# Kernel optimization log

Hardware: AMD Instinct MI355X
Metric: run time of the kernel (lower is better)

The kernel has to match this reference:

```python
import jax, jax.numpy as jnp
import numpy as np

NHEAD = 8
TEMP = 1.0
LAMB = 1.0
G_MIN = 1e-3


def _linear(x, w, b):
    # torch nn.Linear convention: w is (out, in)
    return x @ w.T + b


def _ln(x, s, b):
    m = x.mean(-1, keepdims=True)
    v = ((x - m) ** 2).mean(-1, keepdims=True)
    return (x - m) / jnp.sqrt(v + 1e-5) * s + b


def _gate(x, w, b):
    # UncertaintyGate, gate_mode='mu_times_evi'
    nig = _linear(x, w, b)  # [B, L, 4]
    mu = nig[..., 0]
    v = jax.nn.softplus(nig[..., 1]) + 1e-6
    alpha = jax.nn.softplus(nig[..., 2]) + 1.0 + 1e-6
    beta = jax.nn.softplus(nig[..., 3]) + 1e-6
    sigma_e2 = beta / (v * (alpha - 1.0))
    g = jax.nn.sigmoid(mu) * jnp.exp(-LAMB * sigma_e2)
    return jnp.clip(g, G_MIN, 1.0)  # [B, L]


def _cross_attn(q, k, v, gate, mask):
    B, Lq, D = q.shape
    Lk = k.shape[1]
    hd = D // NHEAD
    q = q.reshape(B, Lq, NHEAD, hd).transpose(0, 2, 1, 3)
    k = k.reshape(B, Lk, NHEAD, hd).transpose(0, 2, 1, 3)
    v = v.reshape(B, Lk, NHEAD, hd).transpose(0, 2, 1, 3)
    scores = jnp.einsum('bhqd,bhkd->bhqk', q, k) / jnp.sqrt(jnp.float32(hd))
    scores = scores + jnp.log(gate + 1e-9)[:, None, None, :]  # per-key log-gate bias
    scores = jnp.where(mask[:, None, None, :] == 0, -1e9, scores)
    attn = jax.nn.softmax(scores / TEMP, axis=-1)
    out = jnp.einsum('bhqk,bhkd->bhqd', attn, v)
    return out.transpose(0, 2, 1, 3).reshape(B, Lq, D)


def _ffn(x, w1, b1, w2, b2):
    return _linear(jax.nn.gelu(_linear(x, w1, b1), approximate=False), w2, b2)


def setup_inputs() -> dict:
    key = jax.random.key(0)
    ks = iter(jax.random.split(key, 64))
    D, B, Ld, Lp = 512, 16, 256, 1024
    def w(shape, s=0.02):
        return jax.random.normal(next(ks), shape, jnp.float32) * s
    inp = {
        'h_d': jax.random.normal(next(ks), (B, Ld, D), jnp.float32),
        'h_p': jax.random.normal(next(ks), (B, Lp, D), jnp.float32),
        'gd_w': w((4, D)), 'gd_b': jnp.zeros((4,), jnp.float32),
        'gp_w': w((4, D)), 'gp_b': jnp.zeros((4,), jnp.float32),
        'wqd_w': w((D, D)), 'wqd_b': jnp.zeros((D,), jnp.float32),
        'wkp_w': w((D, D)), 'wkp_b': jnp.zeros((D,), jnp.float32),
        'wvp_w': w((D, D)), 'wvp_b': jnp.zeros((D,), jnp.float32),
        'wqp_w': w((D, D)), 'wqp_b': jnp.zeros((D,), jnp.float32),
        'wkd_w': w((D, D)), 'wkd_b': jnp.zeros((D,), jnp.float32),
        'wvd_w': w((D, D)), 'wvd_b': jnp.zeros((D,), jnp.float32),
        'od_w': w((D, D)), 'od_b': jnp.zeros((D,), jnp.float32),
        'op_w': w((D, D)), 'op_b': jnp.zeros((D,), jnp.float32),
        'fd1_w': w((4 * D, D)), 'fd1_b': jnp.zeros((4 * D,), jnp.float32),
        'fd2_w': w((D, 4 * D)), 'fd2_b': jnp.zeros((D,), jnp.float32),
        'fp1_w': w((4 * D, D)), 'fp1_b': jnp.zeros((4 * D,), jnp.float32),
        'fp2_w': w((D, 4 * D)), 'fp2_b': jnp.zeros((D,), jnp.float32),
        'nd1_s': jnp.ones((D,), jnp.float32), 'nd1_b': jnp.zeros((D,), jnp.float32),
        'nd2_s': jnp.ones((D,), jnp.float32), 'nd2_b': jnp.zeros((D,), jnp.float32),
        'np1_s': jnp.ones((D,), jnp.float32), 'np1_b': jnp.zeros((D,), jnp.float32),
        'np2_s': jnp.ones((D,), jnp.float32), 'np2_b': jnp.zeros((D,), jnp.float32),
        'mask_d': jnp.ones((B, Ld), jnp.int32),
        'mask_p': jnp.ones((B, Lp), jnp.int32),
    }
    return inp


def reference(h_d, h_p, gd_w, gd_b, gp_w, gp_b, wqd_w, wqd_b, wkp_w, wkp_b,
              wvp_w, wvp_b, wqp_w, wqp_b, wkd_w, wkd_b, wvd_w, wvd_b,
              od_w, od_b, op_w, op_b, fd1_w, fd1_b, fd2_w, fd2_b,
              fp1_w, fp1_b, fp2_w, fp2_b, nd1_s, nd1_b, nd2_s, nd2_b,
              np1_s, np1_b, np2_s, np2_b, mask_d, mask_p):
    # gates are computed from the ORIGINAL inputs
    g_d = _gate(h_d, gd_w, gd_b)
    g_p = _gate(h_p, gp_w, gp_b)
    # drug attends to protein
    attn_d = _cross_attn(_linear(h_d, wqd_w, wqd_b),
                         _linear(h_p, wkp_w, wkp_b),
                         _linear(h_p, wvp_w, wvp_b), g_p, mask_p)
    h_d = _ln(h_d + _linear(attn_d, od_w, od_b), nd1_s, nd1_b)
    # protein attends to UPDATED drug (matches original control flow)
    attn_p = _cross_attn(_linear(h_p, wqp_w, wqp_b),
                         _linear(h_d, wkd_w, wkd_b),
                         _linear(h_d, wvd_w, wvd_b), g_d, mask_d)
    h_p = _ln(h_p + _linear(attn_p, op_w, op_b), np1_s, np1_b)
    h_d = _ln(h_d + _ffn(h_d, fd1_w, fd1_b, fd2_w, fd2_b), nd2_s, nd2_b)
    h_p = _ln(h_p + _ffn(h_p, fp1_w, fp1_b, fp2_w, fp2_b), np2_s, np2_b)
    return (h_d, h_p)
```

## Files before the change

kernel.cpp:

```cpp
#include <hip/hip_runtime.h>

typedef float f32x4 __attribute__((ext_vector_type(4)));
typedef short bfrag __attribute__((ext_vector_type(8)));
typedef short s16x8 __attribute__((ext_vector_type(8)));
typedef unsigned short u16;

__device__ __forceinline__ u16 f2bf(float f) {
  union { float f; unsigned u; } x; x.f = f;
  unsigned r = x.u + 0x7fffu + ((x.u >> 16) & 1u);
  return (u16)(r >> 16);
}
__device__ __forceinline__ float bf2f(u16 v) {
  union { unsigned u; float f; } x; x.u = ((unsigned)v) << 16;
  return x.f;
}

__device__ __forceinline__ void g2l16(const void* g, void* l) {
  void* gnc = const_cast<void*>(g);
  __builtin_amdgcn_global_load_lds((__attribute__((address_space(1))) void*)gnc,
                                   (__attribute__((address_space(3))) void*)l, 16, 0, 0);
}

__device__ __forceinline__ f32x4 mfma16(bfrag a, bfrag b, f32x4 c) {
  asm volatile("v_mfma_f32_16x16x32_bf16 %0, %1, %2, %0" : "+v"(c) : "v"(a), "v"(b));
  return c;
}

__device__ __forceinline__ float wred_sum(float s) {
  #pragma unroll
  for (int o = 32; o; o >>= 1) s += __shfl_xor(s, o);
  return s;
}

struct CvtArgs {
  const float* s[14];
  u16* d[14];
  int eb[14];
};

__global__ __launch_bounds__(256) void cvt_all(CvtArgs a) {
  const int blk = blockIdx.x;
  int base = 0;
  const float* sp = a.s[0];
  u16* dp = a.d[0];
  #pragma unroll
  for (int i = 0; i < 13; ++i) {
    if (blk >= a.eb[i]) { base = a.eb[i]; sp = a.s[i + 1]; dp = a.d[i + 1]; }
  }
  const size_t gi = ((size_t)(blk - base) * 256 + threadIdx.x) * 4;
  float4 f = *(const float4*)(sp + gi);
  ushort4 o;
  o.x = f2bf(f.x); o.y = f2bf(f.y); o.z = f2bf(f.z); o.w = f2bf(f.w);
  *(ushort4*)(dp + gi) = o;
}

__device__ __forceinline__ float softplus_s(float x) {
  return fmaxf(x, 0.f) + log1pf(expf(-fabsf(x)));
}

__global__ __launch_bounds__(256) void gate_k(
    const float* __restrict__ hd, const float* __restrict__ hp,
    const float* __restrict__ wd, const float* __restrict__ bd,
    const float* __restrict__ wp, const float* __restrict__ bp,
    float* __restrict__ lgd, float* __restrict__ lgp, int mdTok) {
  const int lane = threadIdx.x & 63, wv = threadIdx.x >> 6;
  size_t tok = (size_t)blockIdx.x * 4 + wv;
  const float* h; const float* w4; const float* b4; float* lg;
  if (tok < (size_t)mdTok) { h = hd; w4 = wd; b4 = bd; lg = lgd; }
  else { h = hp; w4 = wp; b4 = bp; lg = lgp; tok -= mdTok; }
  const float* x = h + tok * 512;
  float s0 = 0.f, s1 = 0.f, s2 = 0.f, s3 = 0.f;
  #pragma unroll
  for (int i = 0; i < 8; ++i) {
    int c = (i << 6) + lane;
    float xv = x[c];
    s0 += xv * w4[c];
    s1 += xv * w4[512 + c];
    s2 += xv * w4[1024 + c];
    s3 += xv * w4[1536 + c];
  }
  s0 = wred_sum(s0); s1 = wred_sum(s1); s2 = wred_sum(s2); s3 = wred_sum(s3);
  if (lane == 0) {
    float mu = s0 + b4[0];
    float va = softplus_s(s1 + b4[1]) + 1e-6f;
    float al = softplus_s(s2 + b4[2]) + 1.f + 1e-6f;
    float be = softplus_s(s3 + b4[3]) + 1e-6f;
    float se2 = be / (va * (al - 1.f));
    float g = (1.f / (1.f + expf(-mu))) * expf(-se2);
    g = fminf(fmaxf(g, 1e-3f), 1.f);
    lg[tok] = logf(g + 1e-9f);
  }
}

template <int RES, int OUT>
__global__ __launch_bounds__(256) void ln_k(const void* __restrict__ resv,
                                            const u16* __restrict__ y,
                                            const float* __restrict__ sc,
                                            const float* __restrict__ bi,
                                            void* __restrict__ outv) {
  const int lane = threadIdx.x & 63, w = threadIdx.x >> 6;
  const size_t row = (size_t)blockIdx.x * 4 + w;
  const int c0 = lane * 8;
  float v[8];
  s16x8 yv = *(const s16x8*)(y + row * 512 + c0);
  if constexpr (RES == 0) {
    const float* rf = (const float*)resv + row * 512 + c0;
    float4 r0 = *(const float4*)rf, r1 = *(const float4*)(rf + 4);
    v[0] = r0.x; v[1] = r0.y; v[2] = r0.z; v[3] = r0.w;
    v[4] = r1.x; v[5] = r1.y; v[6] = r1.z; v[7] = r1.w;
  } else {
    s16x8 rv = *(const s16x8*)((const u16*)resv + row * 512 + c0);
    #pragma unroll
    for (int i = 0; i < 8; ++i) v[i] = bf2f((u16)rv[i]);
  }
  float s = 0.f;
  #pragma unroll
  for (int i = 0; i < 8; ++i) { v[i] += bf2f((u16)yv[i]); s += v[i]; }
  s = wred_sum(s);
  float m = s * (1.f / 512.f);
  float s2 = 0.f;
  #pragma unroll
  for (int i = 0; i < 8; ++i) { float d = v[i] - m; s2 += d * d; }
  s2 = wred_sum(s2);
  float inv = rsqrtf(s2 * (1.f / 512.f) + 1e-5f);
  float4 sc0 = *(const float4*)(sc + c0), sc1 = *(const float4*)(sc + c0 + 4);
  float4 bi0 = *(const float4*)(bi + c0), bi1 = *(const float4*)(bi + c0 + 4);
  float scv[8] = {sc0.x, sc0.y, sc0.z, sc0.w, sc1.x, sc1.y, sc1.z, sc1.w};
  float biv[8] = {bi0.x, bi0.y, bi0.z, bi0.w, bi1.x, bi1.y, bi1.z, bi1.w};
  float o[8];
  #pragma unroll
  for (int i = 0; i < 8; ++i) o[i] = (v[i] - m) * inv * scv[i] + biv[i];
  if constexpr (OUT == 0) {
    float* of = (float*)outv + row * 512 + c0;
    *(float4*)of = float4{o[0], o[1], o[2], o[3]};
    *(float4*)(of + 4) = float4{o[4], o[5], o[6], o[7]};
  } else {
    s16x8 ov;
    #pragma unroll
    for (int i = 0; i < 8; ++i) ov[i] = (short)f2bf(o[i]);
    *(s16x8*)((u16*)outv + row * 512 + c0) = ov;
  }
}

template <int KT>
__global__ __launch_bounds__(256) void flash_k(
    const u16* __restrict__ Q, const u16* __restrict__ Kv,
    const u16* __restrict__ Vt, const float* __restrict__ logg,
    const int* __restrict__ mask, u16* __restrict__ Out,
    int Lq, int Lk, float scale) {
  __shared__ __align__(16) u16 Kl[KT * 64];
  __shared__ __align__(16) u16 Vl[64 * KT];
  __shared__ __align__(16) u16 Pl[64 * (KT + 8)];
  const int tid = threadIdx.x;
  const int lane = tid & 63, wv = tid >> 6;
  const int lr = lane & 15, lg4 = lane >> 4;
  const int bh = blockIdx.z;
  const int b = bh >> 3, h = bh & 7;
  const int q0 = blockIdx.x * 64;

  bfrag af[2];
  {
    const u16* qrow = Q + (size_t)(b * Lq + q0 + wv * 16 + lr) * 512 + h * 64;
    af[0] = *(const bfrag*)(qrow + lg4 * 8);
    af[1] = *(const bfrag*)(qrow + 32 + lg4 * 8);
  }
  float mreg[4] = {-3e38f, -3e38f, -3e38f, -3e38f};
  float lreg[4] = {0.f, 0.f, 0.f, 0.f};
  f32x4 Oa[4] = {};
  const float* lgb = logg + (size_t)b * Lk;
  const int* mkb = mask + (size_t)b * Lk;

  const int NKT = Lk / KT;
  for (int t = 0; t < NKT; ++t) {
    const int k0 = t * KT;
    __syncthreads();
    {
      const char* kb = (const char*)(Kv + (size_t)(b * Lk + k0) * 512 + h * 64);
      #pragma unroll
      for (int r = 0; r < KT / 32; ++r) {
        int o = r * 4096 + tid * 16;
        int rr = o >> 7, cd = (o >> 4) & 7;
        int cs = cd ^ (rr & 7);
        g2l16(kb + (size_t)rr * 1024 + cs * 16, (char*)Kl + o);
      }
      const char* vb = (const char*)(Vt + (size_t)bh * 64 * Lk + k0);
      #pragma unroll
      for (int r = 0; r < KT / 32; ++r) {
        int o = r * 4096 + tid * 16;
        int rr = o >> 8, cd = (o >> 4) & 15;
        int cs = (cd & 8) | ((cd & 7) ^ (rr & 7));
        g2l16(vb + (size_t)rr * (Lk * 2) + cs * 16, (char*)Vl + o);
      }
    }
    __syncthreads();

    f32x4 sa[KT / 16];
    #pragma unroll
    for (int n = 0; n < KT / 16; ++n) {
      sa[n] = f32x4{0.f, 0.f, 0.f, 0.f};
      int row = n * 16 + lr;
      #pragma unroll
      for (int ks = 0; ks < 2; ++ks) {
        bfrag kf = *(const bfrag*)(Kl + row * 64 + (((ks * 4 + lg4) ^ (row & 7)) * 8));
        sa[n] = mfma16(af[ks], kf, sa[n]);
      }
    }
    asm volatile("s_nop 7\n\ts_nop 7");

    float pv[KT / 16][4];
    float nm[4] = {-3e38f, -3e38f, -3e38f, -3e38f};
    #pragma unroll
    for (int n = 0; n < KT / 16; ++n) {
      int kk = k0 + n * 16 + lr;
      float lgv = lgb[kk];
      int mkv = mkb[kk];
      #pragma unroll
      for (int e = 0; e < 4; ++e) {
        float tv = mkv ? fmaf(sa[n][e], scale, lgv) : -1e9f;
        pv[n][e] = tv;
        nm[e] = fmaxf(nm[e], tv);
      }
    }
    float fac[4], rs[4];
    #pragma unroll
    for (int e = 0; e < 4; ++e) {
      nm[e] = fmaxf(nm[e], __shfl_xor(nm[e], 1));
      nm[e] = fmaxf(nm[e], __shfl_xor(nm[e], 2));
      nm[e] = fmaxf(nm[e], __shfl_xor(nm[e], 4));
      nm[e] = fmaxf(nm[e], __shfl_xor(nm[e], 8));
      nm[e] = fmaxf(nm[e], mreg[e]);
      fac[e] = __expf(mreg[e] - nm[e]);
      mreg[e] = nm[e];
      rs[e] = 0.f;
    }
    #pragma unroll
    for (int n = 0; n < KT / 16; ++n)
      #pragma unroll
      for (int e = 0; e < 4; ++e) {
        float p = __expf(pv[n][e] - nm[e]);
        pv[n][e] = p;
        rs[e] += p;
      }
    #pragma unroll
    for (int e = 0; e < 4; ++e) {
      rs[e] += __shfl_xor(rs[e], 1);
      rs[e] += __shfl_xor(rs[e], 2);
      rs[e] += __shfl_xor(rs[e], 4);
      rs[e] += __shfl_xor(rs[e], 8);
      lreg[e] = lreg[e] * fac[e] + rs[e];
    }
    #pragma unroll
    for (int n2 = 0; n2 < 4; ++n2)
      #pragma unroll
      for (int e = 0; e < 4; ++e) Oa[n2][e] *= fac[e];

    {
      int prow = wv * 16 + lg4 * 4;
      #pragma unroll
      for (int n = 0; n < KT / 16; ++n)
        #pragma unroll
        for (int e = 0; e < 4; ++e)
          Pl[(prow + e) * (KT + 8) + n * 16 + lr] = f2bf(pv[n][e]);
    }
    #pragma unroll
    for (int ks = 0; ks < KT / 32; ++ks) {
      bfrag pf = *(const bfrag*)(Pl + (wv * 16 + lr) * (KT + 8) + (ks * 4 + lg4) * 8);
      #pragma unroll
      for (int n2 = 0; n2 < 4; ++n2) {
        int vrow = n2 * 16 + lr;
        int ch = ks * 4 + lg4;
        int chs = (ch & 8) | ((ch & 7) ^ (vrow & 7));
        bfrag vf = *(const bfrag*)(Vl + vrow * KT + chs * 8);
        Oa[n2] = mfma16(pf, vf, Oa[n2]);
      }
    }
  }
  asm volatile("s_nop 7\n\ts_nop 7");

  float inv[4];
  #pragma unroll
  for (int e = 0; e < 4; ++e) inv[e] = 1.f / lreg[e];
  u16* ob = Out + (size_t)(b * Lq + q0 + wv * 16 + lg4 * 4) * 512 + h * 64;
  #pragma unroll
  for (int n2 = 0; n2 < 4; ++n2)
    #pragma unroll
    for (int e = 0; e < 4; ++e)
      ob[(size_t)e * 512 + n2 * 16 + lr] = f2bf(Oa[n2][e] * inv[e]);
}

template <int FM, int FN, int EPI>
__global__ __launch_bounds__(256) void gemm_k(
    const u16* __restrict__ A, const u16* __restrict__ W,
    const float* __restrict__ bias, void* __restrict__ C,
    int K, int lda, int ldw, int ldc, int NB, int TR) {
  constexpr int BM = 2 * FM * 16;
  constexpr int BN = 2 * FN * 16;
  __shared__ __align__(16) u16 Al[BM * 64];
  __shared__ __align__(16) u16 Wl[BN * 64];
  const int tid = threadIdx.x;
  const int qq = gridDim.x >> 3;
  const int wg = (blockIdx.x & 7) * qq + (blockIdx.x >> 3);
  const int bx = wg % NB, by = wg / NB;
  const int row0 = by * BM, col0 = bx * BN;
  const int lane = tid & 63, wv = tid >> 6;
  const int wr = wv >> 1, wc = wv & 1;
  const int rowW = wr * FM * 16, colW = wc * FN * 16;
  const int lr = lane & 15, lg4 = lane >> 4;

  const u16* aSrc[BM / 32];
  const u16* wSrc[BN / 32];
  int aDst[BM / 32], wDst[BN / 32];
  #pragma unroll
  for (int r = 0; r < BM / 32; ++r) {
    int o = r * 4096 + tid * 16;
    int arow = o >> 7, cd = (o >> 4) & 7, cs = cd ^ (arow & 7);
    aSrc[r] = A + (size_t)(row0 + arow) * lda + cs * 8;
    aDst[r] = o;
  }
  #pragma unroll
  for (int r = 0; r < BN / 32; ++r) {
    int o = r * 4096 + tid * 16;
    int wrow = o >> 7, cd = (o >> 4) & 7, cs = cd ^ (wrow & 7);
    wSrc[r] = W + (size_t)(col0 + wrow) * ldw + cs * 8;
    wDst[r] = o;
  }
  int aOff[FM][2], wOff[FN][2];
  #pragma unroll
  for (int m = 0; m < FM; ++m) {
    int rowi = rowW + m * 16 + lr;
    #pragma unroll
    for (int ks = 0; ks < 2; ++ks)
      aOff[m][ks] = rowi * 64 + (((ks * 4 + lg4) ^ (rowi & 7)) * 8);
  }
  #pragma unroll
  for (int n = 0; n < FN; ++n) {
    int rowi = colW + n * 16 + lr;
    #pragma unroll
    for (int ks = 0; ks < 2; ++ks)
      wOff[n][ks] = rowi * 64 + (((ks * 4 + lg4) ^ (rowi & 7)) * 8);
  }

  f32x4 acc[FM][FN] = {};

  for (int k0 = 0; k0 < K; k0 += 64) {
    #pragma unroll
    for (int r = 0; r < BM / 32; ++r) g2l16(aSrc[r] + k0, (char*)Al + aDst[r]);
    #pragma unroll
    for (int r = 0; r < BN / 32; ++r) g2l16(wSrc[r] + k0, (char*)Wl + wDst[r]);
    __syncthreads();
    #pragma unroll
    for (int ks = 0; ks < 2; ++ks) {
      bfrag af[FM], wf[FN];
      #pragma unroll
      for (int m = 0; m < FM; ++m) af[m] = *(const bfrag*)(Al + aOff[m][ks]);
      #pragma unroll
      for (int n = 0; n < FN; ++n) wf[n] = *(const bfrag*)(Wl + wOff[n][ks]);
      #pragma unroll
      for (int m = 0; m < FM; ++m)
        #pragma unroll
        for (int n = 0; n < FN; ++n) acc[m][n] = mfma16(af[m], wf[n], acc[m][n]);
    }
    __syncthreads();
  }
  asm volatile("s_nop 7\n\ts_nop 7\n\ts_nop 7");

  #pragma unroll
  for (int m = 0; m < FM; ++m) {
    #pragma unroll
    for (int n = 0; n < FN; ++n) {
      int rb = row0 + rowW + m * 16 + lg4 * 4;
      int c = col0 + colW + n * 16 + lr;
      float bv = bias[c];
      if constexpr (EPI == 1) {
        u16* Cu = (u16*)C;
        #pragma unroll
        for (int e = 0; e < 4; ++e)
          Cu[(size_t)(rb + e) * ldc + c] = f2bf(acc[m][n][e] + bv);
      } else if constexpr (EPI == 2) {
        u16* Cu = (u16*)C;
        #pragma unroll
        for (int e = 0; e < 4; ++e) {
          float vv = acc[m][n][e] + bv;
          float gl = 0.5f * vv * (1.f + erff(vv * 0.70710678118f));
          Cu[(size_t)(rb + e) * ldc + c] = f2bf(gl);
        }
      } else {
        u16* Cu = (u16*)C;
        int b2 = rb / TR, j0 = rb - b2 * TR;
        int h2 = c >> 6, dd = c & 63;
        ushort4 pk;
        pk.x = f2bf(acc[m][n][0] + bv);
        pk.y = f2bf(acc[m][n][1] + bv);
        pk.z = f2bf(acc[m][n][2] + bv);
        pk.w = f2bf(acc[m][n][3] + bv);
        *(ushort4*)&Cu[(((size_t)b2 * 8 + h2) * 64 + dd) * TR + j0] = pk;
      }
    }
  }
}

extern "C" void kernel_launch(void* const* d_in, const int* in_sizes, int n_in,
                              void* d_out, int out_size, void* d_ws, size_t ws_size,
                              hipStream_t stream) {
  const float* h_d = (const float*)d_in[0];
  const float* h_p = (const float*)d_in[1];
  const float* gd_w = (const float*)d_in[2];
  const float* gd_b = (const float*)d_in[3];
  const float* gp_w = (const float*)d_in[4];
  const float* gp_b = (const float*)d_in[5];
  const float* wqd_w = (const float*)d_in[6];  const float* wqd_b = (const float*)d_in[7];
  const float* wkp_w = (const float*)d_in[8];  const float* wkp_b = (const float*)d_in[9];
  const float* wvp_w = (const float*)d_in[10]; const float* wvp_b = (const float*)d_in[11];
  const float* wqp_w = (const float*)d_in[12]; const float* wqp_b = (const float*)d_in[13];
  const float* wkd_w = (const float*)d_in[14]; const float* wkd_b = (const float*)d_in[15];
  const float* wvd_w = (const float*)d_in[16]; const float* wvd_b = (const float*)d_in[17];
  const float* od_w = (const float*)d_in[18];  const float* od_b = (const float*)d_in[19];
  const float* op_w = (const float*)d_in[20];  const float* op_b = (const float*)d_in[21];
  const float* fd1_w = (const float*)d_in[22]; const float* fd1_b = (const float*)d_in[23];
  const float* fd2_w = (const float*)d_in[24]; const float* fd2_b = (const float*)d_in[25];
  const float* fp1_w = (const float*)d_in[26]; const float* fp1_b = (const float*)d_in[27];
  const float* fp2_w = (const float*)d_in[28]; const float* fp2_b = (const float*)d_in[29];
  const float* nd1_s = (const float*)d_in[30]; const float* nd1_b = (const float*)d_in[31];
  const float* nd2_s = (const float*)d_in[32]; const float* nd2_b = (const float*)d_in[33];
  const float* np1_s = (const float*)d_in[34]; const float* np1_b = (const float*)d_in[35];
  const float* np2_s = (const float*)d_in[36]; const float* np2_b = (const float*)d_in[37];
  const int* mask_d = (const int*)d_in[38];
  const int* mask_p = (const int*)d_in[39];

  constexpr int B = 16, Ld = 256, Lp = 1024, D = 512, H = 8, F = 2048;
  constexpr int Md = B * Ld;
  constexpr int Mp = B * Lp;
  constexpr int BH = B * H;

  char* ws = (char*)d_ws;
  size_t off = 0;
  auto alloc = [&](size_t bytes) {
    size_t o = off;
    off += (bytes + 255) & ~(size_t)255;
    return o;
  };
  auto a16 = [&](size_t els) { return (u16*)(ws + alloc(els * 2)); };
  auto a32 = [&](size_t els) { return (float*)(ws + alloc(els * 4)); };

  u16* w_qd = a16((size_t)D * D);
  u16* w_kp = a16((size_t)D * D);
  u16* w_vp = a16((size_t)D * D);
  u16* w_qp = a16((size_t)D * D);
  u16* w_kd = a16((size_t)D * D);
  u16* w_vd = a16((size_t)D * D);
  u16* w_od = a16((size_t)D * D);
  u16* w_op = a16((size_t)D * D);
  u16* w_fd1 = a16((size_t)F * D);
  u16* w_fd2 = a16((size_t)F * D);
  u16* w_fp1 = a16((size_t)F * D);
  u16* w_fp2 = a16((size_t)F * D);

  u16* hd16 = a16((size_t)Md * D);
  u16* hd2_16 = a16((size_t)Md * D);
  u16* hp16 = a16((size_t)Mp * D);
  u16* qd16 = a16((size_t)Md * D);
  u16* kp16 = a16((size_t)Mp * D);
  u16* vt16 = a16((size_t)Mp * D);
  u16* obuf16 = a16((size_t)Mp * D);
  u16* t16 = a16((size_t)Mp * F);
  float* logg_d = a32(Md);
  float* logg_p = a32(Mp);

  {
    CvtArgs a;
    const float* src[14] = {h_d, h_p, wqd_w, wkp_w, wvp_w, wqp_w, wkd_w,
                            wvd_w, od_w, op_w, fd1_w, fd2_w, fp1_w, fp2_w};
    u16* dst[14] = {hd16, hp16, w_qd, w_kp, w_vp, w_qp, w_kd,
                    w_vd, w_od, w_op, w_fd1, w_fd2, w_fp1, w_fp2};
    const int nelem[14] = {Md * D, Mp * D, D * D, D * D, D * D, D * D, D * D,
                           D * D, D * D, D * D, F * D, F * D, F * D, F * D};
    int pfx = 0;
    for (int i = 0; i < 14; ++i) {
      a.s[i] = src[i];
      a.d[i] = dst[i];
      pfx += nelem[i] / 1024;
      a.eb[i] = pfx;
    }
    cvt_all<<<pfx, 256, 0, stream>>>(a);
  }

  gate_k<<<(Md + Mp) / 4, 256, 0, stream>>>(h_d, h_p, gd_w, gd_b, gp_w, gp_b,
                                            logg_d, logg_p, Md);

  gemm_k<4, 4, 1><<<(Md / 128) * (D / 128), 256, 0, stream>>>(
      hd16, w_qd, wqd_b, qd16, D, D, D, D, D / 128, 0);
  gemm_k<4, 4, 1><<<(Mp / 128) * (D / 128), 256, 0, stream>>>(
      hp16, w_kp, wkp_b, kp16, D, D, D, D, D / 128, 0);
  gemm_k<4, 4, 3><<<(Mp / 128) * (D / 128), 256, 0, stream>>>(
      hp16, w_vp, wvp_b, vt16, D, D, D, 0, D / 128, Lp);

  flash_k<128><<<dim3(Ld / 64, 1, BH), 256, 0, stream>>>(
      qd16, kp16, vt16, logg_p, mask_p, hd16, Ld, Lp, 0.125f);

  gemm_k<4, 4, 1><<<(Md / 128) * (D / 128), 256, 0, stream>>>(
      hd16, w_od, od_b, obuf16, D, D, D, D, D / 128, 0);
  ln_k<0, 1><<<Md / 4, 256, 0, stream>>>(h_d, obuf16, nd1_s, nd1_b, hd2_16);

  gemm_k<4, 4, 1><<<(Mp / 128) * (D / 128), 256, 0, stream>>>(
      hp16, w_qp, wqp_b, kp16, D, D, D, D, D / 128, 0);
  gemm_k<4, 4, 1><<<(Md / 128) * (D / 128), 256, 0, stream>>>(
      hd2_16, w_kd, wkd_b, qd16, D, D, D, D, D / 128, 0);
  gemm_k<4, 4, 3><<<(Md / 128) * (D / 128), 256, 0, stream>>>(
      hd2_16, w_vd, wvd_b, vt16, D, D, D, 0, D / 128, Ld);

  flash_k<128><<<dim3(Lp / 64, 1, BH), 256, 0, stream>>>(
      kp16, qd16, vt16, logg_d, mask_d, hp16, Lp, Ld, 0.125f);

  gemm_k<4, 4, 1><<<(Mp / 128) * (D / 128), 256, 0, stream>>>(
      hp16, w_op, op_b, obuf16, D, D, D, D, D / 128, 0);
  ln_k<0, 1><<<Mp / 4, 256, 0, stream>>>(h_p, obuf16, np1_s, np1_b, hp16);

  gemm_k<4, 4, 2><<<(Md / 128) * (F / 128), 256, 0, stream>>>(
      hd2_16, w_fd1, fd1_b, t16, D, D, D, F, F / 128, 0);
  gemm_k<4, 4, 1><<<(Md / 128) * (D / 128), 256, 0, stream>>>(
      t16, w_fd2, fd2_b, obuf16, F, F, F, D, D / 128, 0);
  ln_k<1, 0><<<Md / 4, 256, 0, stream>>>(hd2_16, obuf16, nd2_s, nd2_b, (float*)d_out);

  gemm_k<4, 4, 2><<<(Mp / 128) * (F / 128), 256, 0, stream>>>(
      hp16, w_fp1, fp1_b, t16, D, D, D, F, F / 128, 0);
  gemm_k<4, 4, 1><<<(Mp / 128) * (D / 128), 256, 0, stream>>>(
      t16, w_fp2, fp2_b, obuf16, F, F, F, D, D / 128, 0);
  ln_k<1, 0><<<Mp / 4, 256, 0, stream>>>(hp16, obuf16, np2_s, np2_b,
                                         (float*)d_out + (size_t)Md * D);
}
```

Baseline: 390.3 us.

## Fuse protein K/V/Q and drug K/V projections into wide GEMMs with 256x256 tiles

Concatenates the protein-side K, V and Q projection weights and biases into one 1536-wide GEMM, and the drug-side K and V into one 1024-wide GEMM. Multi-output epilogues write a row-major output and a transposed V layout. A new 512-thread 256x256-tile GEMM with double-buffered global-to-LDS loads and an interleaved MFMA schedule is used for the large protein projections and the protein FFN up-projection. This cuts kernel launches and re-reads of the activations, at the cost of relying on adjacent weight buffers being contiguous and on a more complex pipelined kernel.

```diff
diff --git a/kernel.cpp b/kernel.cpp
--- a/kernel.cpp
+++ b/kernel.cpp
@@ -30,6 +30,10 @@
   #pragma unroll
   for (int o = 32; o; o >>= 1) s += __shfl_xor(s, o);
   return s;
+}
+
+__device__ __forceinline__ float gelu_f(float v) {
+  return 0.5f * v * (1.f + erff(v * 0.70710678118f));
 }
 
 struct CvtArgs {
@@ -52,6 +56,19 @@
   ushort4 o;
   o.x = f2bf(f.x); o.y = f2bf(f.y); o.z = f2bf(f.z); o.w = f2bf(f.w);
   *(ushort4*)(dp + gi) = o;
+}
+
+__global__ __launch_bounds__(512) void biascat_k(
+    const float* __restrict__ bkp, const float* __restrict__ bvp,
+    const float* __restrict__ bqp, const float* __restrict__ bkd,
+    const float* __restrict__ bvd, float* __restrict__ bp3,
+    float* __restrict__ bd2) {
+  int t = threadIdx.x;
+  bp3[t] = bkp[t];
+  bp3[512 + t] = bvp[t];
+  bp3[1024 + t] = bqp[t];
+  bd2[t] = bkd[t];
+  bd2[512 + t] = bvd[t];
 }
 
 __device__ __forceinline__ float softplus_s(float x) {
@@ -291,7 +308,7 @@
 template <int FM, int FN, int EPI>
 __global__ __launch_bounds__(256) void gemm_k(
     const u16* __restrict__ A, const u16* __restrict__ W,
-    const float* __restrict__ bias, void* __restrict__ C,
+    const float* __restrict__ bias, void* __restrict__ C, void* __restrict__ C2,
     int K, int lda, int ldw, int ldc, int NB, int TR) {
   constexpr int BM = 2 * FM * 16;
   constexpr int BN = 2 * FN * 16;
@@ -379,12 +396,9 @@
       } else if constexpr (EPI == 2) {
         u16* Cu = (u16*)C;
         #pragma unroll
-        for (int e = 0; e < 4; ++e) {
-          float vv = acc[m][n][e] + bv;
-          float gl = 0.5f * vv * (1.f + erff(vv * 0.70710678118f));
-          Cu[(size_t)(rb + e) * ldc + c] = f2bf(gl);
-        }
-      } else {
+        for (int e = 0; e < 4; ++e)
+          Cu[(size_t)(rb + e) * ldc + c] = f2bf(gelu_f(acc[m][n][e] + bv));
+      } else if constexpr (EPI == 3) {
         u16* Cu = (u16*)C;
         int b2 = rb / TR, j0 = rb - b2 * TR;
         int h2 = c >> 6, dd = c & 63;
@@ -394,9 +408,190 @@
         pk.z = f2bf(acc[m][n][2] + bv);
         pk.w = f2bf(acc[m][n][3] + bv);
         *(ushort4*)&Cu[(((size_t)b2 * 8 + h2) * 64 + dd) * TR + j0] = pk;
+      } else {
+        if (c < 512) {
+          u16* Cu = (u16*)C;
+          #pragma unroll
+          for (int e = 0; e < 4; ++e)
+            Cu[(size_t)(rb + e) * ldc + c] = f2bf(acc[m][n][e] + bv);
+        } else {
+          u16* Cu = (u16*)C2;
+          int cl = c - 512;
+          int b2 = rb / TR, j0 = rb - b2 * TR;
+          int h2 = cl >> 6, dd = cl & 63;
+          ushort4 pk;
+          pk.x = f2bf(acc[m][n][0] + bv);
+          pk.y = f2bf(acc[m][n][1] + bv);
+          pk.z = f2bf(acc[m][n][2] + bv);
+          pk.w = f2bf(acc[m][n][3] + bv);
+          *(ushort4*)&Cu[(((size_t)b2 * 8 + h2) * 64 + dd) * TR + j0] = pk;
+        }
       }
     }
   }
+}
+
+#define GBAR asm volatile("s_barrier" ::: "memory")
+template <int EPI>
+__global__ __launch_bounds__(512, 1) void gemm8_k(
+    const u16* __restrict__ A, const u16* __restrict__ W,
+    const float* __restrict__ bias, void* __restrict__ C, void* __restrict__ C2,
+    void* __restrict__ C3, int K, int lda, int ldw, int ldc, int NB, int TR) {
+  __shared__ __align__(16) u16 Ab[2][2][128 * 64];
+  __shared__ __align__(16) u16 Bb[2][2][128 * 64];
+  const int tid = threadIdx.x;
+  const int qq = gridDim.x >> 3;
+  const int wg = (blockIdx.x & 7) * qq + (blockIdx.x >> 3);
+  const int bx = wg % NB, by = wg / NB;
+  const int row0 = by * 256, col0 = bx * 256;
+  const int lane = tid & 63, wv = tid >> 6;
+  const int wr = wv >> 2, wc = wv & 3;
+  const int lr = lane & 15, lg4 = lane >> 4;
+  const int NT = K >> 6;
+
+  const int srow = tid >> 3;
+  const int scs = (tid & 7) ^ (srow & 7);
+  const u16* aS[2][2];
+  const u16* wS[2][2];
+  #pragma unroll
+  for (int h = 0; h < 2; ++h)
+    #pragma unroll
+    for (int i = 0; i < 2; ++i) {
+      int r = i * 64 + srow;
+      aS[h][i] = A + (size_t)(row0 + h * 128 + r) * lda + scs * 8;
+      wS[h][i] = W + (size_t)(col0 + h * 128 + r) * ldw + scs * 8;
+    }
+  const int dstoff = tid * 16;
+
+  auto stA = [&](int buf, int h, int tt) {
+    if (tt < NT) {
+      char* d = (char*)&Ab[buf][h][0];
+      g2l16(aS[h][0] + tt * 64, d + dstoff);
+      g2l16(aS[h][1] + tt * 64, d + 8192 + dstoff);
+    }
+  };
+  auto stB = [&](int buf, int h, int tt) {
+    if (tt < NT) {
+      char* d = (char*)&Bb[buf][h][0];
+      g2l16(wS[h][0] + tt * 64, d + dstoff);
+      g2l16(wS[h][1] + tt * 64, d + 8192 + dstoff);
+    }
+  };
+
+  const u16* Abase[2] = {&Ab[0][wr][0], &Ab[1][wr][0]};
+  const u16* Bbase[2] = {&Bb[0][wc >> 1][0], &Bb[1][wc >> 1][0]};
+  int cko[2];
+  #pragma unroll
+  for (int kk = 0; kk < 2; ++kk) cko[kk] = ((kk * 4 + lg4) ^ (lr & 7)) * 8;
+  const int brow0 = (wc & 1) * 64;
+
+  f32x4 acc[8][4] = {};
+  bfrag ar[4][2], b0r[2][2], b1r[2][2];
+
+#define LDA8(buf, qm)                                                     \
+  {                                                                       \
+    const u16* _b = Abase[buf];                                           \
+    _Pragma("unroll") for (int m = 0; m < 4; ++m) {                       \
+      int ro = (((qm) * 4 + m) * 16 + lr) * 64;                           \
+      ar[m][0] = *(const bfrag*)(_b + ro + cko[0]);                       \
+      ar[m][1] = *(const bfrag*)(_b + ro + cko[1]);                       \
+    }                                                                     \
+  }
+#define LDB8(buf, qn, br)                                                 \
+  {                                                                       \
+    const u16* _b = Bbase[buf];                                           \
+    _Pragma("unroll") for (int n = 0; n < 2; ++n) {                       \
+      int ro = (brow0 + ((qn) * 2 + n) * 16 + lr) * 64;                   \
+      br[n][0] = *(const bfrag*)(_b + ro + cko[0]);                       \
+      br[n][1] = *(const bfrag*)(_b + ro + cko[1]);                       \
+    }                                                                     \
+  }
+#define MM8(qm, qn, br)                                                   \
+  {                                                                       \
+    __builtin_amdgcn_s_setprio(1);                                        \
+    _Pragma("unroll") for (int m = 0; m < 4; ++m)                         \
+        _Pragma("unroll") for (int n = 0; n < 2; ++n) {                   \
+      acc[(qm) * 4 + m][(qn) * 2 + n] =                                   \
+          mfma16(ar[m][0], br[n][0], acc[(qm) * 4 + m][(qn) * 2 + n]);    \
+      acc[(qm) * 4 + m][(qn) * 2 + n] =                                   \
+          mfma16(ar[m][1], br[n][1], acc[(qm) * 4 + m][(qn) * 2 + n]);    \
+    }                                                                     \
+    __builtin_amdgcn_s_setprio(0);                                        \
+  }
+
+  stB(0, 0, 0); stB(0, 1, 0); stA(0, 0, 0); stA(0, 1, 0);
+  stB(1, 0, 1); stB(1, 1, 1); stA(1, 0, 1);
+  asm volatile("s_waitcnt vmcnt(6)" ::: "memory");
+  GBAR;
+
+  const int NI = NT >> 1;
+  for (int j = 0; j < NI; ++j) {
+    const int t2 = 2 * j + 2, t3 = 2 * j + 3;
+    const bool last = (j == NI - 1);
+    LDA8(0, 0); LDB8(0, 0, b0r); stA(1, 1, 2 * j + 1);
+    GBAR; MM8(0, 0, b0r); GBAR;
+    LDB8(0, 1, b1r); stB(0, 0, t2);
+    GBAR; MM8(0, 1, b1r); GBAR;
+    LDA8(0, 1); stB(0, 1, t2);
+    GBAR; MM8(1, 1, b1r); GBAR;
+    stA(0, 0, t2);
+    if (last) asm volatile("s_waitcnt vmcnt(0)" ::: "memory");
+    else      asm volatile("s_waitcnt vmcnt(6)" ::: "memory");
+    GBAR; MM8(1, 0, b0r); GBAR;
+    LDA8(1, 0); LDB8(1, 0, b0r); stA(0, 1, t2);
+    GBAR; MM8(0, 0, b0r); GBAR;
+    LDB8(1, 1, b1r); stB(1, 0, t3);
+    GBAR; MM8(0, 1, b1r); GBAR;
+    LDA8(1, 1); stB(1, 1, t3);
+    GBAR; MM8(1, 1, b1r); GBAR;
+    stA(1, 0, t3);
+    if (!last) asm volatile("s_waitcnt vmcnt(6)" ::: "memory");
+    GBAR; MM8(1, 0, b0r); GBAR;
+  }
+  asm volatile("s_nop 7\n\ts_nop 7\n\ts_nop 7");
+
+  #pragma unroll
+  for (int mf = 0; mf < 8; ++mf) {
+    #pragma unroll
+    for (int nf = 0; nf < 4; ++nf) {
+      int rb = row0 + wr * 128 + mf * 16 + lg4 * 4;
+      int c = col0 + wc * 64 + nf * 16 + lr;
+      float bv = bias[c];
+      if constexpr (EPI == 2) {
+        u16* Cu = (u16*)C;
+        #pragma unroll
+        for (int e = 0; e < 4; ++e)
+          Cu[(size_t)(rb + e) * ldc + c] = f2bf(gelu_f(acc[mf][nf][e] + bv));
+      } else {
+        if (c < 512) {
+          u16* Cu = (u16*)C;
+          #pragma unroll
+          for (int e = 0; e < 4; ++e)
+            Cu[(size_t)(rb + e) * 512 + c] = f2bf(acc[mf][nf][e] + bv);
+        } else if (c < 1024) {
+          u16* Cu = (u16*)C2;
+          int cl = c - 512;
+          int b2 = rb / TR, j0 = rb - b2 * TR;
+          int h2 = cl >> 6, dd = cl & 63;
+          ushort4 pk;
+          pk.x = f2bf(acc[mf][nf][0] + bv);
+          pk.y = f2bf(acc[mf][nf][1] + bv);
+          pk.z = f2bf(acc[mf][nf][2] + bv);
+          pk.w = f2bf(acc[mf][nf][3] + bv);
+          *(ushort4*)&Cu[(((size_t)b2 * 8 + h2) * 64 + dd) * TR + j0] = pk;
+        } else {
+          u16* Cu = (u16*)C3;
+          int cl = c - 1024;
+          #pragma unroll
+          for (int e = 0; e < 4; ++e)
+            Cu[(size_t)(rb + e) * 512 + cl] = f2bf(acc[mf][nf][e] + bv);
+        }
+      }
+    }
+  }
+#undef LDA8
+#undef LDB8
+#undef MM8
 }
 
 extern "C" void kernel_launch(void* const* d_in, const int* in_sizes, int n_in,
@@ -460,11 +655,14 @@
   u16* hp16 = a16((size_t)Mp * D);
   u16* qd16 = a16((size_t)Md * D);
   u16* kp16 = a16((size_t)Mp * D);
+  u16* qp16 = a16((size_t)Mp * D);
   u16* vt16 = a16((size_t)Mp * D);
   u16* obuf16 = a16((size_t)Mp * D);
   u16* t16 = a16((size_t)Mp * F);
   float* logg_d = a32(Md);
   float* logg_p = a32(Mp);
+  float* bp3 = a32(1536);
+  float* bd2 = a32(1024);
 
   {
     CvtArgs a;
@@ -483,48 +681,44 @@
     }
     cvt_all<<<pfx, 256, 0, stream>>>(a);
   }
+  biascat_k<<<1, 512, 0, stream>>>(wkp_b, wvp_b, wqp_b, wkd_b, wvd_b, bp3, bd2);
 
   gate_k<<<(Md + Mp) / 4, 256, 0, stream>>>(h_d, h_p, gd_w, gd_b, gp_w, gp_b,
                                             logg_d, logg_p, Md);
 
+  gemm8_k<4><<<(Mp / 256) * (1536 / 256), 512, 0, stream>>>(
+      hp16, w_kp, bp3, kp16, vt16, qp16, D, D, D, 0, 1536 / 256, Lp);
+
   gemm_k<4, 4, 1><<<(Md / 128) * (D / 128), 256, 0, stream>>>(
-      hd16, w_qd, wqd_b, qd16, D, D, D, D, D / 128, 0);
-  gemm_k<4, 4, 1><<<(Mp / 128) * (D / 128), 256, 0, stream>>>(
-      hp16, w_kp, wkp_b, kp16, D, D, D, D, D / 128, 0);
-  gemm_k<4, 4, 3><<<(Mp / 128) * (D / 128), 256, 0, stream>>>(
-      hp16, w_vp, wvp_b, vt16, D, D, D, 0, D / 128, Lp);
+      hd16, w_qd, wqd_b, qd16, nullptr, D, D, D, D, D / 128, 0);
 
   flash_k<128><<<dim3(Ld / 64, 1, BH), 256, 0, stream>>>(
       qd16, kp16, vt16, logg_p, mask_p, hd16, Ld, Lp, 0.125f);
 
   gemm_k<4, 4, 1><<<(Md / 128) * (D / 128), 256, 0, stream>>>(
-      hd16, w_od, od_b, obuf16, D, D, D, D, D / 128, 0);
+      hd16, w_od, od_b, obuf16, nullptr, D, D, D, D, D / 128, 0);
   ln_k<0, 1><<<Md / 4, 256, 0, stream>>>(h_d, obuf16, nd1_s, nd1_b, hd2_16);
 
+  gemm_k<4, 4, 5><<<(Md / 128) * (1024 / 128), 256, 0, stream>>>(
+      hd2_16, w_kd, bd2, qd16, vt16, D, D, D, D, 1024 / 128, Ld);
+
+  flash_k<128><<<dim3(Lp / 64, 1, BH), 256, 0, stream>>>(
+      qp16, qd16, vt16, logg_d, mask_d, hp16, Lp, Ld, 0.125f);
+
   gemm_k<4, 4, 1><<<(Mp / 128) * (D / 128), 256, 0, stream>>>(
-      hp16, w_qp, wqp_b, kp16, D, D, D, D, D / 128, 0);
+      hp16, w_op, op_b, obuf16, nullptr, D, D, D, D, D / 128, 0);
+  ln_k<0, 1><<<Mp / 4, 256, 0, stream>>>(h_p, obuf16, np1_s, np1_b, hp16);
+
+  gemm_k<4, 4, 2><<<(Md / 128) * (F / 128), 256, 0, stream>>>(
+      hd2_16, w_fd1, fd1_b, t16, nullptr, D, D, D, F, F / 128, 0);
   gemm_k<4, 4, 1><<<(Md / 128) * (D / 128), 256, 0, stream>>>(
-      hd2_16, w_kd, wkd_b, qd16, D, D, D, D, D / 128, 0);
-  gemm_k<4, 4, 3><<<(Md / 128) * (D / 128), 256, 0, stream>>>(
-      hd2_16, w_vd, wvd_b, vt16, D, D, D, 0, D / 128, Ld);
-
-  flash_k<128><<<dim3(Lp / 64, 1, BH), 256, 0, stream>>>(
-      kp16, qd16, vt16, logg_d, mask_d, hp16, Lp, Ld, 0.125f);
-
+      t16, w_fd2, fd2_b, obuf16, nullptr, F, F, F, D, D / 128, 0);
+  ln_k<1, 0><<<Md / 4, 256, 0, stream>>>(hd2_16, obuf16, nd2_s, nd2_b, (float*)d_out);
+
+  gemm8_k<2><<<(Mp / 256) * (F / 256), 512, 0, stream>>>(
+      hp16, w_fp1, fp1_b, t16, nullptr, nullptr, D, D, D, F, F / 256, 0);
   gemm_k<4, 4, 1><<<(Mp / 128) * (D / 128), 256, 0, stream>>>(
-      hp16, w_op, op_b, obuf16, D, D, D, D, D / 128, 0);
-  ln_k<0, 1><<<Mp / 4, 256, 0, stream>>>(h_p, obuf16, np1_s, np1_b, hp16);
-
-  gemm_k<4, 4, 2><<<(Md / 128) * (F / 128), 256, 0, stream>>>(
-      hd2_16, w_fd1, fd1_b, t16, D, D, D, F, F / 128, 0);
-  gemm_k<4, 4, 1><<<(Md / 128) * (D / 128), 256, 0, stream>>>(
-      t16, w_fd2, fd2_b, obuf16, F, F, F, D, D / 128, 0);
-  ln_k<1, 0><<<Md / 4, 256, 0, stream>>>(hd2_16, obuf16, nd2_s, nd2_b, (float*)d_out);
-
-  gemm_k<4, 4, 2><<<(Mp / 128) * (F / 128), 256, 0, stream>>>(
-      hp16, w_fp1, fp1_b, t16, D, D, D, F, F / 128, 0);
-  gemm_k<4, 4, 1><<<(Mp / 128) * (D / 128), 256, 0, stream>>>(
-      t16, w_fp2, fp2_b, obuf16, F, F, F, D, D / 128, 0);
+      t16, w_fp2, fp2_b, obuf16, nullptr, F, F, F, D, D / 128, 0);
   ln_k<1, 0><<<Mp / 4, 256, 0, stream>>>(hp16, obuf16, np2_s, np2_b,
                                          (float*)d_out + (size_t)Md * D);
 }
```

New measurement: 513.8 us. 1.32x slower.

## Fuse same-input projection GEMMs into wide GEMMs with split epilogues

Applied to the files above, without the earlier changes.

The K, V and Q projections of h_p become one GEMM with N=1536, and the K and V projections of the updated h_d become one GEMM with N=1024. New epilogue modes route each column range to its own output buffer, including the transposed V layout. A small kernel concatenates the biases, and the fused GEMMs rely on the converted weight buffers sitting next to each other in memory. The first LayerNorm residual now reads the bf16 copy instead of fp32, and the trailing barrier after the last k-step is skipped. Together these cut launches and repeated reads of A tiles, at some cost in residual precision.

```diff
diff --git a/kernel.cpp b/kernel.cpp
--- a/kernel.cpp
+++ b/kernel.cpp
@@ -30,6 +30,10 @@
   #pragma unroll
   for (int o = 32; o; o >>= 1) s += __shfl_xor(s, o);
   return s;
+}
+
+__device__ __forceinline__ float gelu_f(float v) {
+  return 0.5f * v * (1.f + erff(v * 0.70710678118f));
 }
 
 struct CvtArgs {
@@ -52,6 +56,19 @@
   ushort4 o;
   o.x = f2bf(f.x); o.y = f2bf(f.y); o.z = f2bf(f.z); o.w = f2bf(f.w);
   *(ushort4*)(dp + gi) = o;
+}
+
+__global__ __launch_bounds__(512) void biascat_k(
+    const float* __restrict__ bkp, const float* __restrict__ bvp,
+    const float* __restrict__ bqp, const float* __restrict__ bkd,
+    const float* __restrict__ bvd, float* __restrict__ bp3,
+    float* __restrict__ bd2) {
+  int t = threadIdx.x;
+  bp3[t] = bkp[t];
+  bp3[512 + t] = bvp[t];
+  bp3[1024 + t] = bqp[t];
+  bd2[t] = bkd[t];
+  bd2[512 + t] = bvd[t];
 }
 
 __device__ __forceinline__ float softplus_s(float x) {
@@ -92,8 +109,8 @@
   }
 }
 
-template <int RES, int OUT>
-__global__ __launch_bounds__(256) void ln_k(const void* __restrict__ resv,
+template <int OUT>
+__global__ __launch_bounds__(256) void ln_k(const u16* __restrict__ res,
                                             const u16* __restrict__ y,
                                             const float* __restrict__ sc,
                                             const float* __restrict__ bi,
@@ -103,19 +120,13 @@
   const int c0 = lane * 8;
   float v[8];
   s16x8 yv = *(const s16x8*)(y + row * 512 + c0);
-  if constexpr (RES == 0) {
-    const float* rf = (const float*)resv + row * 512 + c0;
-    float4 r0 = *(const float4*)rf, r1 = *(const float4*)(rf + 4);
-    v[0] = r0.x; v[1] = r0.y; v[2] = r0.z; v[3] = r0.w;
-    v[4] = r1.x; v[5] = r1.y; v[6] = r1.z; v[7] = r1.w;
-  } else {
-    s16x8 rv = *(const s16x8*)((const u16*)resv + row * 512 + c0);
-    #pragma unroll
-    for (int i = 0; i < 8; ++i) v[i] = bf2f((u16)rv[i]);
-  }
+  s16x8 rv = *(const s16x8*)(res + row * 512 + c0);
   float s = 0.f;
   #pragma unroll
-  for (int i = 0; i < 8; ++i) { v[i] += bf2f((u16)yv[i]); s += v[i]; }
+  for (int i = 0; i < 8; ++i) {
+    v[i] = bf2f((u16)rv[i]) + bf2f((u16)yv[i]);
+    s += v[i];
+  }
   s = wred_sum(s);
   float m = s * (1.f / 512.f);
   float s2 = 0.f;
@@ -291,8 +302,8 @@
 template <int FM, int FN, int EPI>
 __global__ __launch_bounds__(256) void gemm_k(
     const u16* __restrict__ A, const u16* __restrict__ W,
-    const float* __restrict__ bias, void* __restrict__ C,
-    int K, int lda, int ldw, int ldc, int NB, int TR) {
+    const float* __restrict__ bias, void* __restrict__ C, void* __restrict__ C2,
+    void* __restrict__ C3, int K, int lda, int ldw, int ldc, int NB, int TR) {
   constexpr int BM = 2 * FM * 16;
   constexpr int BN = 2 * FN * 16;
   __shared__ __align__(16) u16 Al[BM * 64];
@@ -360,7 +371,7 @@
         #pragma unroll
         for (int n = 0; n < FN; ++n) acc[m][n] = mfma16(af[m], wf[n], acc[m][n]);
     }
-    __syncthreads();
+    if (k0 + 64 < K) __syncthreads();
   }
   asm volatile("s_nop 7\n\ts_nop 7\n\ts_nop 7");
 
@@ -379,21 +390,50 @@
       } else if constexpr (EPI == 2) {
         u16* Cu = (u16*)C;
         #pragma unroll
-        for (int e = 0; e < 4; ++e) {
-          float vv = acc[m][n][e] + bv;
-          float gl = 0.5f * vv * (1.f + erff(vv * 0.70710678118f));
-          Cu[(size_t)(rb + e) * ldc + c] = f2bf(gl);
+        for (int e = 0; e < 4; ++e)
+          Cu[(size_t)(rb + e) * ldc + c] = f2bf(gelu_f(acc[m][n][e] + bv));
+      } else if constexpr (EPI == 4) {
+        if (c < 512) {
+          u16* Cu = (u16*)C;
+          #pragma unroll
+          for (int e = 0; e < 4; ++e)
+            Cu[(size_t)(rb + e) * 512 + c] = f2bf(acc[m][n][e] + bv);
+        } else if (c < 1024) {
+          u16* Cu = (u16*)C2;
+          int cl = c - 512;
+          int b2 = rb / TR, j0 = rb - b2 * TR;
+          int h2 = cl >> 6, dd = cl & 63;
+          ushort4 pk;
+          pk.x = f2bf(acc[m][n][0] + bv);
+          pk.y = f2bf(acc[m][n][1] + bv);
+          pk.z = f2bf(acc[m][n][2] + bv);
+          pk.w = f2bf(acc[m][n][3] + bv);
+          *(ushort4*)&Cu[(((size_t)b2 * 8 + h2) * 64 + dd) * TR + j0] = pk;
+        } else {
+          u16* Cu = (u16*)C3;
+          int cl = c - 1024;
+          #pragma unroll
+          for (int e = 0; e < 4; ++e)
+            Cu[(size_t)(rb + e) * 512 + cl] = f2bf(acc[m][n][e] + bv);
         }
       } else {
-        u16* Cu = (u16*)C;
-        int b2 = rb / TR, j0 = rb - b2 * TR;
-        int h2 = c >> 6, dd = c & 63;
-        ushort4 pk;
-        pk.x = f2bf(acc[m][n][0] + bv);
-        pk.y = f2bf(acc[m][n][1] + bv);
-        pk.z = f2bf(acc[m][n][2] + bv);
-        pk.w = f2bf(acc[m][n][3] + bv);
-        *(ushort4*)&Cu[(((size_t)b2 * 8 + h2) * 64 + dd) * TR + j0] = pk;
+        if (c < 512) {
+          u16* Cu = (u16*)C;
+          #pragma unroll
+          for (int e = 0; e < 4; ++e)
+            Cu[(size_t)(rb + e) * ldc + c] = f2bf(acc[m][n][e] + bv);
+        } else {
+          u16* Cu = (u16*)C2;
+          int cl = c - 512;
+          int b2 = rb / TR, j0 = rb - b2 * TR;
+          int h2 = cl >> 6, dd = cl & 63;
+          ushort4 pk;
+          pk.x = f2bf(acc[m][n][0] + bv);
+          pk.y = f2bf(acc[m][n][1] + bv);
+          pk.z = f2bf(acc[m][n][2] + bv);
+          pk.w = f2bf(acc[m][n][3] + bv);
+          *(ushort4*)&Cu[(((size_t)b2 * 8 + h2) * 64 + dd) * TR + j0] = pk;
+        }
       }
     }
   }
@@ -460,11 +500,14 @@
   u16* hp16 = a16((size_t)Mp * D);
   u16* qd16 = a16((size_t)Md * D);
   u16* kp16 = a16((size_t)Mp * D);
+  u16* qp16 = a16((size_t)Mp * D);
   u16* vt16 = a16((size_t)Mp * D);
   u16* obuf16 = a16((size_t)Mp * D);
   u16* t16 = a16((size_t)Mp * F);
   float* logg_d = a32(Md);
   float* logg_p = a32(Mp);
+  float* bp3 = a32(1536);
+  float* bd2 = a32(1024);
 
   {
     CvtArgs a;
@@ -483,48 +526,44 @@
     }
     cvt_all<<<pfx, 256, 0, stream>>>(a);
   }
+  biascat_k<<<1, 512, 0, stream>>>(wkp_b, wvp_b, wqp_b, wkd_b, wvd_b, bp3, bd2);
 
   gate_k<<<(Md + Mp) / 4, 256, 0, stream>>>(h_d, h_p, gd_w, gd_b, gp_w, gp_b,
                                             logg_d, logg_p, Md);
 
+  gemm_k<4, 4, 4><<<(Mp / 128) * (1536 / 128), 256, 0, stream>>>(
+      hp16, w_kp, bp3, kp16, vt16, qp16, D, D, D, D, 1536 / 128, Lp);
+
   gemm_k<4, 4, 1><<<(Md / 128) * (D / 128), 256, 0, stream>>>(
-      hd16, w_qd, wqd_b, qd16, D, D, D, D, D / 128, 0);
+      hd16, w_qd, wqd_b, qd16, nullptr, nullptr, D, D, D, D, D / 128, 0);
+
+  flash_k<128><<<dim3(Ld / 64, 1, BH), 256, 0, stream>>>(
+      qd16, kp16, vt16, logg_p, mask_p, qd16, Ld, Lp, 0.125f);
+
+  gemm_k<4, 4, 1><<<(Md / 128) * (D / 128), 256, 0, stream>>>(
+      qd16, w_od, od_b, obuf16, nullptr, nullptr, D, D, D, D, D / 128, 0);
+  ln_k<1><<<Md / 4, 256, 0, stream>>>(hd16, obuf16, nd1_s, nd1_b, hd2_16);
+
+  gemm_k<4, 4, 5><<<(Md / 128) * (1024 / 128), 256, 0, stream>>>(
+      hd2_16, w_kd, bd2, qd16, vt16, nullptr, D, D, D, D, 1024 / 128, Ld);
+
+  flash_k<128><<<dim3(Lp / 64, 1, BH), 256, 0, stream>>>(
+      qp16, qd16, vt16, logg_d, mask_d, qp16, Lp, Ld, 0.125f);
+
   gemm_k<4, 4, 1><<<(Mp / 128) * (D / 128), 256, 0, stream>>>(
-      hp16, w_kp, wkp_b, kp16, D, D, D, D, D / 128, 0);
-  gemm_k<4, 4, 3><<<(Mp / 128) * (D / 128), 256, 0, stream>>>(
-      hp16, w_vp, wvp_b, vt16, D, D, D, 0, D / 128, Lp);
-
-  flash_k<128><<<dim3(Ld / 64, 1, BH), 256, 0, stream>>>(
-      qd16, kp16, vt16, logg_p, mask_p, hd16, Ld, Lp, 0.125f);
-
+      qp16, w_op, op_b, obuf16, nullptr, nullptr, D, D, D, D, D / 128, 0);
+  ln_k<1><<<Mp / 4, 256, 0, stream>>>(hp16, obuf16, np1_s, np1_b, hp16);
+
+  gemm_k<4, 4, 2><<<(Md / 128) * (F / 128), 256, 0, stream>>>(
+      hd2_16, w_fd1, fd1_b, t16, nullptr, nullptr, D, D, D, F, F / 128, 0);
   gemm_k<4, 4, 1><<<(Md / 128) * (D / 128), 256, 0, stream>>>(
-      hd16, w_od, od_b, obuf16, D, D, D, D, D / 128, 0);
-  ln_k<0, 1><<<Md / 4, 256, 0, stream>>>(h_d, obuf16, nd1_s, nd1_b, hd2_16);
-
+      t16, w_fd2, fd2_b, obuf16, nullptr, nullptr, F, F, F, D, D / 128, 0);
+  ln_k<0><<<Md / 4, 256, 0, stream>>>(hd2_16, obuf16, nd2_s, nd2_b, (float*)d_out);
+
+  gemm_k<4, 4, 2><<<(Mp / 128) * (F / 128), 256, 0, stream>>>(
+      hp16, w_fp1, fp1_b, t16, nullptr, nullptr, D, D, D, F, F / 128, 0);
   gemm_k<4, 4, 1><<<(Mp / 128) * (D / 128), 256, 0, stream>>>(
-      hp16, w_qp, wqp_b, kp16, D, D, D, D, D / 128, 0);
-  gemm_k<4, 4, 1><<<(Md / 128) * (D / 128), 256, 0, stream>>>(
-      hd2_16, w_kd, wkd_b, qd16, D, D, D, D, D / 128, 0);
-  gemm_k<4, 4, 3><<<(Md / 128) * (D / 128), 256, 0, stream>>>(
-      hd2_16, w_vd, wvd_b, vt16, D, D, D, 0, D / 128, Ld);
-
-  flash_k<128><<<dim3(Lp / 64, 1, BH), 256, 0, stream>>>(
-      kp16, qd16, vt16, logg_d, mask_d, hp16, Lp, Ld, 0.125f);
-
-  gemm_k<4, 4, 1><<<(Mp / 128) * (D / 128), 256, 0, stream>>>(
-      hp16, w_op, op_b, obuf16, D, D, D, D, D / 128, 0);
-  ln_k<0, 1><<<Mp / 4, 256, 0, stream>>>(h_p, obuf16, np1_s, np1_b, hp16);
-
-  gemm_k<4, 4, 2><<<(Md / 128) * (F / 128), 256, 0, stream>>>(
-      hd2_16, w_fd1, fd1_b, t16, D, D, D, F, F / 128, 0);
-  gemm_k<4, 4, 1><<<(Md / 128) * (D / 128), 256, 0, stream>>>(
-      t16, w_fd2, fd2_b, obuf16, F, F, F, D, D / 128, 0);
-  ln_k<1, 0><<<Md / 4, 256, 0, stream>>>(hd2_16, obuf16, nd2_s, nd2_b, (float*)d_out);
-
-  gemm_k<4, 4, 2><<<(Mp / 128) * (F / 128), 256, 0, stream>>>(
-      hp16, w_fp1, fp1_b, t16, D, D, D, F, F / 128, 0);
-  gemm_k<4, 4, 1><<<(Mp / 128) * (D / 128), 256, 0, stream>>>(
-      t16, w_fp2, fp2_b, obuf16, F, F, F, D, D / 128, 0);
-  ln_k<1, 0><<<Mp / 4, 256, 0, stream>>>(hp16, obuf16, np2_s, np2_b,
-                                         (float*)d_out + (size_t)Md * D);
-}
+      t16, w_fp2, fp2_b, obuf16, nullptr, nullptr, F, F, F, D, D / 128, 0);
+  ln_k<0><<<Mp / 4, 256, 0, stream>>>(hp16, obuf16, np2_s, np2_b,
+                                      (float*)d_out + (size_t)Md * D);
+}
```

Result: no change. 396.5 us (+1.6%).
